# Kernel tuning notes

Measured on AMD Instinct MI355X. Metric: run time of the kernel, lower is better.

## Reference

```python
import jax, jax.numpy as jnp
import numpy as np

DIM = 1024
HEADS = 16
HEAD_DIM = 64
ROT = 32          # rotary_emb_dim = min(max(head_dim//2, 32), head_dim)
BASE = 10000.0
SEQ = 2048
BATCH = 2


def setup_inputs() -> dict:
    key = jax.random.key(0)
    k1, k2, k3, k4 = jax.random.split(key, 4)
    s = 0.02
    return {
        "x": jax.random.normal(k1, (BATCH, SEQ, DIM), dtype=jnp.float32),
        # Linear weights stored as [in, out] (equivalent to torch W^T)
        "w_q": jax.random.normal(k2, (DIM, HEADS * HEAD_DIM), dtype=jnp.float32) * s,
        "w_kv": jax.random.normal(k3, (DIM, 2 * HEADS * HEAD_DIM), dtype=jnp.float32) * s,
        "w_out": jax.random.normal(k4, (HEADS * HEAD_DIM, DIM), dtype=jnp.float32) * s,
    }


def _rotate_half(t):
    # x-transformers style: split last dim in half, (-x2, x1)
    x1, x2 = t[..., : ROT // 2], t[..., ROT // 2 :]
    return jnp.concatenate([-x2, x1], axis=-1)


def _apply_rope(t, cos, sin):
    # rotate only the first ROT dims of head_dim, pass through the rest
    t_rot, t_pass = t[..., :ROT], t[..., ROT:]
    t_rot = t_rot * cos + _rotate_half(t_rot) * sin
    return jnp.concatenate([t_rot, t_pass], axis=-1)


def reference(x, w_q, w_kv, w_out):
    b, n, _ = x.shape
    # QKV projections
    q = (x @ w_q).reshape(b, n, HEADS, HEAD_DIM).transpose(0, 2, 1, 3)  # b h n d
    k, v = jnp.split(x @ w_kv, 2, axis=-1)
    k = k.reshape(b, n, HEADS, HEAD_DIM).transpose(0, 2, 1, 3)
    v = v.reshape(b, n, HEADS, HEAD_DIM).transpose(0, 2, 1, 3)

    # rotary embedding over full kv length (no cache -> k.shape[-2] == n)
    inv_freq = 1.0 / (BASE ** (jnp.arange(0, ROT, 2, dtype=jnp.float32) / ROT))
    freqs = jnp.arange(n, dtype=jnp.float32)[:, None] * inv_freq[None, :]  # [n, ROT/2]
    freqs = jnp.concatenate([freqs, freqs], axis=-1)                        # [n, ROT]
    cos, sin = jnp.cos(freqs), jnp.sin(freqs)
    q = _apply_rope(q, cos, sin)
    k = _apply_rope(k, cos, sin)

    # causal attention
    scale = HEAD_DIM ** -0.5
    scores = jnp.einsum('bhid,bhjd->bhij', q, k) * scale  # [b,h,n,n]
    causal_mask = jnp.tril(jnp.ones((n, n), dtype=bool))
    scores = jnp.where(causal_mask, scores, jnp.finfo(scores.dtype).min)
    attn = jax.nn.softmax(scores, axis=-1)
    out = jnp.einsum('bhij,bhjd->bhid', attn, v)

    out = out.transpose(0, 2, 1, 3).reshape(b, n, HEADS * HEAD_DIM)
    return out @ w_out
```

## Files before the change

### kernel.cpp

```cpp
#include <hip/hip_runtime.h>

typedef unsigned short u16;
typedef unsigned int u32;
typedef __bf16 bf16x8 __attribute__((ext_vector_type(8)));
typedef unsigned short u16x8v __attribute__((ext_vector_type(8)));
typedef unsigned short u16x4v __attribute__((ext_vector_type(4)));
typedef unsigned int u32x4 __attribute__((ext_vector_type(4)));
typedef float f32x4 __attribute__((ext_vector_type(4)));
typedef float f32x16 __attribute__((ext_vector_type(16)));

#define SEQ 2048
#define NH 16
#define HD 64
#define DIMM 1024

__device__ __forceinline__ u16 f2bf(float f) {
  unsigned u = __builtin_bit_cast(unsigned, f);
  u += 0x7fffu + ((u >> 16) & 1u);
  return (u16)(u >> 16);
}
__device__ __forceinline__ float bf2f(u16 b) {
  return __builtin_bit_cast(float, ((unsigned)b) << 16);
}
__device__ __forceinline__ u32 pk2(float a, float b) {
  return (u32)f2bf(a) | ((u32)f2bf(b) << 16);
}

__device__ __forceinline__ void gload16(const u16* g, u16* l) {
  __builtin_amdgcn_global_load_lds(
      (const __attribute__((address_space(1))) unsigned int*)g,
      (__attribute__((address_space(3))) unsigned int*)l, 16, 0, 0);
}

__global__ void conv_x(const float* __restrict__ x, u16* __restrict__ oh) {
  size_t i = (size_t)blockIdx.x * 256 + threadIdx.x;
  f32x4 v = *(const f32x4*)(x + i * 4);
  u16x4v h;
#pragma unroll
  for (int j = 0; j < 4; ++j) h[j] = f2bf(v[j]);
  *(u16x4v*)(oh + i * 4) = h;
}

__global__ void conv_wT(const float* __restrict__ W, u16* __restrict__ Wt,
                        int Kd, int Nd) {
  __shared__ float t[32][33];
  int n0 = blockIdx.x * 32, k0 = blockIdx.y * 32;
  int c = threadIdx.x & 31, r8 = threadIdx.x >> 5;
#pragma unroll
  for (int rr = 0; rr < 32; rr += 8)
    t[r8 + rr][c] = W[(size_t)(k0 + r8 + rr) * Nd + n0 + c];
  __syncthreads();
#pragma unroll
  for (int rr = 0; rr < 32; rr += 8)
    Wt[(size_t)(n0 + r8 + rr) * Kd + k0 + c] = f2bf(t[c][r8 + rr]);
}

__global__ void __launch_bounds__(256, 2)
gemmQKV(const u16* __restrict__ Ah, const u16* __restrict__ Bt,
        u16* __restrict__ Qb, u16* __restrict__ Kb, u16* __restrict__ Vb,
        int M, int N, int K) {
  __shared__ u16 AsH[128][64];
  __shared__ u16 BsH[128][64];
  const int tid = threadIdx.x;
  const int lane = tid & 63, wave = tid >> 6;
  const int wr = wave >> 1, wc = wave & 1;
  const int lr = lane & 15, lg = lane >> 4;
  const int bm = blockIdx.y * 128, bn = blockIdx.x * 128;
  const int lrow = lane >> 3;
  const int lcol8 = (lane & 7) * 8;

  f32x4 acc[4][4];
#pragma unroll
  for (int m = 0; m < 4; ++m)
#pragma unroll
    for (int n = 0; n < 4; ++n) acc[m][n] = (f32x4){0.f, 0.f, 0.f, 0.f};

  for (int k0 = 0; k0 < K; k0 += 64) {
    __syncthreads();
#pragma unroll
    for (int c = 0; c < 4; ++c) {
      int r0 = wave * 32 + c * 8;
      size_t arow = (size_t)(bm + r0 + lrow) * K + k0 + lcol8;
      size_t brow = (size_t)(bn + r0 + lrow) * K + k0 + lcol8;
      gload16(Ah + arow, &AsH[r0][0]);
      gload16(Bt + brow, &BsH[r0][0]);
    }
    __syncthreads();
#pragma unroll
    for (int kk = 0; kk < 2; ++kk) {
      bf16x8 afh[4], bfh[4];
#pragma unroll
      for (int m = 0; m < 4; ++m)
        afh[m] = *(const bf16x8*)&AsH[wr * 64 + m * 16 + lr][kk * 32 + lg * 8];
#pragma unroll
      for (int n = 0; n < 4; ++n)
        bfh[n] = *(const bf16x8*)&BsH[wc * 64 + n * 16 + lr][kk * 32 + lg * 8];
#pragma unroll
      for (int m = 0; m < 4; ++m)
#pragma unroll
        for (int n = 0; n < 4; ++n)
          acc[m][n] = __builtin_amdgcn_mfma_f32_16x16x32_bf16(afh[m], bfh[n],
                                                              acc[m][n], 0, 0, 0);
    }
  }

  const int sel = bn >> 10;
  u16* __restrict__ dst = sel == 0 ? Qb : (sel == 1 ? Kb : Vb);
  if (sel < 2) {
    float inv = __expf(-(float)lr * 0.5756462732485115f);
#pragma unroll
    for (int m = 0; m < 4; ++m) {
#pragma unroll
      for (int r = 0; r < 4; ++r) {
        int row = bm + wr * 64 + m * 16 + 4 * lg + r;
        int s = row & (SEQ - 1);
        float ang = (float)s * inv;
        float sn, cs;
        __sincosf(ang, &sn, &cs);
        float x1 = acc[m][0][r], x2 = acc[m][1][r];
        acc[m][0][r] = x1 * cs - x2 * sn;
        acc[m][1][r] = x2 * cs + x1 * sn;
      }
    }
  }

#pragma unroll
  for (int m = 0; m < 4; ++m) {
#pragma unroll
    for (int n = 0; n < 4; ++n) {
#pragma unroll
      for (int r = 0; r < 4; ++r) {
        int row = bm + wr * 64 + m * 16 + 4 * lg + r;
        int col = bn + wc * 64 + n * 16 + lr;
        int b = row >> 11, s = row & 2047;
        int h = (col >> 6) & 15, d = col & 63;
        dst[(((size_t)(b * NH + h)) * SEQ + s) * HD + d] = f2bf(acc[m][n][r]);
      }
    }
  }
}

__global__ void __launch_bounds__(256, 2)
gemm1(const u16* __restrict__ A, const u16* __restrict__ Bt,
      float* __restrict__ CF, int M, int N, int K) {
  __shared__ u16 As[128][64];
  __shared__ u16 Bs[64][64];
  const int tid = threadIdx.x;
  const int lane = tid & 63, wave = tid >> 6;
  const int wr = wave >> 1, wc = wave & 1;
  const int lr = lane & 15, lg = lane >> 4;
  const int bm = blockIdx.y * 128, bn = blockIdx.x * 64;
  const int lrow = lane >> 3;
  const int lcol8 = (lane & 7) * 8;

  f32x4 acc[4][2];
#pragma unroll
  for (int m = 0; m < 4; ++m)
#pragma unroll
    for (int n = 0; n < 2; ++n) acc[m][n] = (f32x4){0.f, 0.f, 0.f, 0.f};

  for (int k0 = 0; k0 < K; k0 += 64) {
    __syncthreads();
#pragma unroll
    for (int c = 0; c < 4; ++c) {
      int r0 = wave * 32 + c * 8;
      gload16(A + (size_t)(bm + r0 + lrow) * K + k0 + lcol8, &As[r0][0]);
    }
#pragma unroll
    for (int c = 0; c < 2; ++c) {
      int r0 = wave * 16 + c * 8;
      gload16(Bt + (size_t)(bn + r0 + lrow) * K + k0 + lcol8, &Bs[r0][0]);
    }
    __syncthreads();
#pragma unroll
    for (int kk = 0; kk < 2; ++kk) {
      bf16x8 af[4], bfr[2];
#pragma unroll
      for (int m = 0; m < 4; ++m)
        af[m] = *(const bf16x8*)&As[wr * 64 + m * 16 + lr][kk * 32 + lg * 8];
#pragma unroll
      for (int n = 0; n < 2; ++n)
        bfr[n] = *(const bf16x8*)&Bs[wc * 32 + n * 16 + lr][kk * 32 + lg * 8];
#pragma unroll
      for (int m = 0; m < 4; ++m)
#pragma unroll
        for (int n = 0; n < 2; ++n)
          acc[m][n] = __builtin_amdgcn_mfma_f32_16x16x32_bf16(af[m], bfr[n],
                                                              acc[m][n], 0, 0, 0);
    }
  }

#pragma unroll
  for (int m = 0; m < 4; ++m)
#pragma unroll
    for (int n = 0; n < 2; ++n)
#pragma unroll
      for (int r = 0; r < 4; ++r) {
        int row = bm + wr * 64 + m * 16 + 4 * lg + r;
        int col = bn + wc * 32 + n * 16 + lr;
        CF[(size_t)row * N + col] = acc[m][n][r];
      }
}

__global__ void __launch_bounds__(512, 1)
attn_kernel(const u16* __restrict__ Q, const u16* __restrict__ K,
            const u16* __restrict__ V, float* __restrict__ Op0,
            float* __restrict__ Op1, float* __restrict__ ml) {
  __shared__ u16 Ks[2][64][72];
  __shared__ u16 Vt[2][64][72];
  const int tid = threadIdx.x, lane = tid & 63, wave = tid >> 6;
  const int g = wave >> 2, w4 = wave & 3;
  const int hi = lane >> 5, l31 = lane & 31;
  const int tid_g = w4 * 64 + lane;
  const int bx = blockIdx.x, bh = blockIdx.y;
  const size_t kvbase = (size_t)bh * SEQ * HD;
  const int HS = 32 * SEQ;
  const int kr0 = tid_g >> 3, kc0 = (tid_g & 7) * 8;
  const int vr = tid_g & 63;
  const int vc0A = (tid_g >> 6) * 8, vc0B = vc0A + 32;

  u16x8v kreg0, kreg1, vreg0, vreg1;
  float* __restrict__ Opart = g ? Op1 : Op0;

#pragma unroll 1
  for (int phase = 0; phase < 2; ++phase) {
    const int qt = phase ? 15 - bx : bx;
    const int nper = qt + 1;
    const int ktbegin = g * nper;
    const int qrow = qt * 128 + w4 * 32 + l31;

    const u16* qp = Q + kvbase + (size_t)qrow * HD + 8 * hi;
    bf16x8 qf0 = *(const bf16x8*)(qp);
    bf16x8 qf1 = *(const bf16x8*)(qp + 16);
    bf16x8 qf2 = *(const bf16x8*)(qp + 32);
    bf16x8 qf3 = *(const bf16x8*)(qp + 48);

    f32x16 o0 = {0.f}, o1 = {0.f};
    float m = -1e30f, l = 0.f;

    {
      const u16* kp = K + kvbase + (size_t)(ktbegin * 64) * HD;
      const u16* vp = V + kvbase + (size_t)(ktbegin * 64) * HD;
      kreg0 = *(const u16x8v*)(kp + (size_t)kr0 * HD + kc0);
      kreg1 = *(const u16x8v*)(kp + (size_t)(kr0 + 32) * HD + kc0);
      vreg0 = *(const u16x8v*)(vp + (size_t)vr * HD + vc0A);
      vreg1 = *(const u16x8v*)(vp + (size_t)vr * HD + vc0B);
    }

#pragma unroll 1
    for (int i = 0; i < nper; ++i) {
      const int kt = ktbegin + i;
      __syncthreads();
      *(u16x8v*)&Ks[g][kr0][kc0] = kreg0;
      *(u16x8v*)&Ks[g][kr0 + 32][kc0] = kreg1;
#pragma unroll
      for (int j = 0; j < 8; ++j) Vt[g][vc0A + j][vr] = vreg0[j];
#pragma unroll
      for (int j = 0; j < 8; ++j) Vt[g][vc0B + j][vr] = vreg1[j];
      __syncthreads();
      if (i + 1 < nper) {
        const u16* kp = K + kvbase + (size_t)((kt + 1) * 64) * HD;
        const u16* vp = V + kvbase + (size_t)((kt + 1) * 64) * HD;
        kreg0 = *(const u16x8v*)(kp + (size_t)kr0 * HD + kc0);
        kreg1 = *(const u16x8v*)(kp + (size_t)(kr0 + 32) * HD + kc0);
        vreg0 = *(const u16x8v*)(vp + (size_t)vr * HD + vc0A);
        vreg1 = *(const u16x8v*)(vp + (size_t)vr * HD + vc0B);
      }

      f32x16 s0 = {0.f}, s1 = {0.f};
      __builtin_amdgcn_s_setprio(1);
#pragma unroll
      for (int kk = 0; kk < 4; ++kk) {
        bf16x8 qk = kk == 0 ? qf0 : (kk == 1 ? qf1 : (kk == 2 ? qf2 : qf3));
        bf16x8 af0 = *(const bf16x8*)&Ks[g][l31][16 * kk + 8 * hi];
        bf16x8 af1 = *(const bf16x8*)&Ks[g][32 + l31][16 * kk + 8 * hi];
        s0 = __builtin_amdgcn_mfma_f32_32x32x16_bf16(af0, qk, s0, 0, 0, 0);
        s1 = __builtin_amdgcn_mfma_f32_32x32x16_bf16(af1, qk, s1, 0, 0, 0);
      }
      __builtin_amdgcn_s_setprio(0);
      s0 *= 0.125f;
      s1 *= 0.125f;

      if (kt >= 2 * qt) {
#pragma unroll
        for (int r = 0; r < 16; ++r) {
          int rowi = (r & 3) + 8 * (r >> 2) + 4 * hi;
          if (kt * 64 + rowi > qrow) s0[r] = -1e30f;
          if (kt * 64 + 32 + rowi > qrow) s1[r] = -1e30f;
        }
      }

      float mx = s0[0];
#pragma unroll
      for (int r = 1; r < 16; ++r) mx = fmaxf(mx, s0[r]);
#pragma unroll
      for (int r = 0; r < 16; ++r) mx = fmaxf(mx, s1[r]);
      mx = fmaxf(mx, __shfl_xor(mx, 32));

      bool defer = __all(mx - m <= 8.f);
      if (!defer) {
        float mn = fmaxf(m, mx);
        float fac = __expf(m - mn);
        m = mn;
        l *= fac;
        o0 *= fac;
        o1 *= fac;
      }
      float rsum = 0.f;
#pragma unroll
      for (int r = 0; r < 16; ++r) {
        s0[r] = __expf(s0[r] - m);
        rsum += s0[r];
      }
#pragma unroll
      for (int r = 0; r < 16; ++r) {
        s1[r] = __expf(s1[r] - m);
        rsum += s1[r];
      }
      rsum += __shfl_xor(rsum, 32);
      l += rsum;

      u32 P0a[4], P1a[4], P0b[4], P1b[4];
#pragma unroll
      for (int gg = 0; gg < 4; ++gg) {
        P0a[gg] = pk2(s0[4 * gg], s0[4 * gg + 1]);
        P1a[gg] = pk2(s0[4 * gg + 2], s0[4 * gg + 3]);
        P0b[gg] = pk2(s1[4 * gg], s1[4 * gg + 1]);
        P1b[gg] = pk2(s1[4 * gg + 2], s1[4 * gg + 3]);
      }

      __builtin_amdgcn_s_setprio(1);
#pragma unroll
      for (int c = 0; c < 4; ++c) {
        const int gA = 2 * (c & 1);
        u32 p0lo, p0hi, p1lo, p1hi;
        if (c < 2) {
          p0lo = P0a[gA];
          p0hi = P0a[gA + 1];
          p1lo = P1a[gA];
          p1hi = P1a[gA + 1];
        } else {
          p0lo = P0b[gA];
          p0hi = P0b[gA + 1];
          p1lo = P1b[gA];
          p1hi = P1b[gA + 1];
        }
        u32 send0 = hi ? p0lo : p0hi;
        u32 send1 = hi ? p1lo : p1hi;
        u32 recv0 = (u32)__shfl_xor((int)send0, 32);
        u32 recv1 = (u32)__shfl_xor((int)send1, 32);
        u32 own0 = hi ? p0hi : p0lo;
        u32 own1 = hi ? p1hi : p1lo;
        u32x4 bw;
        bw[0] = hi ? recv0 : own0;
        bw[1] = hi ? recv1 : own1;
        bw[2] = hi ? own0 : recv0;
        bw[3] = hi ? own1 : recv1;
        bf16x8 bfrag = __builtin_bit_cast(bf16x8, bw);
        bf16x8 av0 = *(const bf16x8*)&Vt[g][l31][16 * c + 8 * hi];
        bf16x8 av1 = *(const bf16x8*)&Vt[g][32 + l31][16 * c + 8 * hi];
        o0 = __builtin_amdgcn_mfma_f32_32x32x16_bf16(av0, bfrag, o0, 0, 0, 0);
        o1 = __builtin_amdgcn_mfma_f32_32x32x16_bf16(av1, bfrag, o1, 0, 0, 0);
      }
      __builtin_amdgcn_s_setprio(0);
    }

    {
      size_t base = ((size_t)bh * SEQ + qrow) * HD;
#pragma unroll
      for (int gg = 0; gg < 4; ++gg) {
        f32x4 v0 = {o0[4 * gg], o0[4 * gg + 1], o0[4 * gg + 2], o0[4 * gg + 3]};
        f32x4 v1 = {o1[4 * gg], o1[4 * gg + 1], o1[4 * gg + 2], o1[4 * gg + 3]};
        *(f32x4*)(Opart + base + 8 * gg + 4 * hi) = v0;
        *(f32x4*)(Opart + base + 32 + 8 * gg + 4 * hi) = v1;
      }
      if (hi == 0) {
        ml[g * HS + bh * SEQ + qrow] = m;
        ml[2 * HS + g * HS + bh * SEQ + qrow] = l;
      }
    }
    __syncthreads();
  }
}

__global__ void merge_kernel(const float* __restrict__ Op0,
                             const float* __restrict__ Op1,
                             const float* __restrict__ ml,
                             u16* __restrict__ O) {
  int i = blockIdx.x * 256 + threadIdx.x;
  int row = i >> 4;
  int d0 = (i & 15) * 4;
  size_t base = (size_t)row * 64 + d0;
  f32x4 o1 = *(const f32x4*)(Op0 + base);
  f32x4 o2 = *(const f32x4*)(Op1 + base);
  const int HS = 32 * SEQ;
  float m1 = ml[row], m2 = ml[HS + row];
  float l1 = ml[2 * HS + row], l2 = ml[3 * HS + row];
  float M = fmaxf(m1, m2);
  float w1 = __expf(m1 - M), w2 = __expf(m2 - M);
  float inv = 1.0f / (l1 * w1 + l2 * w2);
  int bh = row >> 11, s = row & 2047;
  int b = bh >> 4, h = bh & 15;
  u16x4v rr;
#pragma unroll
  for (int j = 0; j < 4; ++j) rr[j] = f2bf((o1[j] * w1 + o2[j] * w2) * inv);
  *(u16x4v*)(O + ((size_t)(b * SEQ + s)) * DIMM + h * HD + d0) = rr;
}

extern "C" void kernel_launch(void* const* d_in, const int* in_sizes, int n_in,
                              void* d_out, int out_size, void* d_ws, size_t ws_size,
                              hipStream_t stream) {
  const float* x = (const float*)d_in[0];
  const float* wq = (const float*)d_in[1];
  const float* wkv = (const float*)d_in[2];
  const float* wout = (const float*)d_in[3];
  float* out = (float*)d_out;

  u16* ws = (u16*)d_ws;
  const size_t M1 = (size_t)1024 * 1024;
  u16* xh = ws;
  u16* xl = xh + 4 * M1;
  u16* wqTh = xl + 4 * M1;
  u16* wkvTh = wqTh + M1;
  u16* Qb = wkvTh + 2 * M1;
  u16* Kb = Qb + 4 * M1;
  u16* Vb = Kb + 4 * M1;
  float* Op0 = out;
  float* Op1 = (float*)xh;
  float* mlbuf = (float*)wqTh;
  u16* Ob = Qb;
  u16* woutT = Kb;

  conv_x<<<4096, 256, 0, stream>>>(x, xh);
  conv_wT<<<dim3(32, 32), 256, 0, stream>>>(wq, wqTh, 1024, 1024);
  conv_wT<<<dim3(64, 32), 256, 0, stream>>>(wkv, wkvTh, 1024, 2048);

  gemmQKV<<<dim3(24, 32), 256, 0, stream>>>(xh, wqTh, Qb, Kb, Vb,
                                            4096, 3072, 1024);

  attn_kernel<<<dim3(8, 32), 512, 0, stream>>>(Qb, Kb, Vb, Op0, Op1, mlbuf);
  merge_kernel<<<4096, 256, 0, stream>>>(Op0, Op1, mlbuf, Ob);

  conv_wT<<<dim3(32, 32), 256, 0, stream>>>(wout, woutT, 1024, 1024);
  gemm1<<<dim3(16, 32), 256, 0, stream>>>(Ob, woutT, out, 4096, 1024, 1024);
}
```

Measured before the change: 129.7 us.

## Split attention into independent per-half blocks instead of paired-phase 512-thread blocks

The attention kernel used to run 512-thread blocks holding two 4-wave groups, each group covering one half of the KV range, with every block handling two mirrored query tiles in sequence to balance causal work. Now each 256-thread block handles one query tile and one KV half, launched on a 16x2x32 grid with launch bounds allowing 4 blocks per CU. This gives 1024 smaller blocks and lets the hardware scheduler do the balancing and overlap, in place of the manual mirrored-tile pairing. The cost is that the explicit load balancing is dropped, so uneven causal tiles depend on the scheduler, and the tighter launch bound may constrain registers.

```diff
diff --git a/kernel.cpp b/kernel.cpp
--- a/kernel.cpp
+++ b/kernel.cpp
@@ -202,184 +202,176 @@
       }
 }
 
-__global__ void __launch_bounds__(512, 1)
+__global__ void __launch_bounds__(256, 4)
 attn_kernel(const u16* __restrict__ Q, const u16* __restrict__ K,
             const u16* __restrict__ V, float* __restrict__ Op0,
             float* __restrict__ Op1, float* __restrict__ ml) {
-  __shared__ u16 Ks[2][64][72];
-  __shared__ u16 Vt[2][64][72];
+  __shared__ u16 Ks[64][72];
+  __shared__ u16 Vt[64][72];
   const int tid = threadIdx.x, lane = tid & 63, wave = tid >> 6;
-  const int g = wave >> 2, w4 = wave & 3;
   const int hi = lane >> 5, l31 = lane & 31;
-  const int tid_g = w4 * 64 + lane;
-  const int bx = blockIdx.x, bh = blockIdx.y;
+  const int qt = blockIdx.x, g = blockIdx.y, bh = blockIdx.z;
   const size_t kvbase = (size_t)bh * SEQ * HD;
   const int HS = 32 * SEQ;
-  const int kr0 = tid_g >> 3, kc0 = (tid_g & 7) * 8;
-  const int vr = tid_g & 63;
-  const int vc0A = (tid_g >> 6) * 8, vc0B = vc0A + 32;
+  const int kr0 = tid >> 3, kc0 = (tid & 7) * 8;
+  const int vr = tid & 63;
+  const int vc0A = (tid >> 6) * 8, vc0B = vc0A + 32;
+
+  const int nper = qt + 1;
+  const int ktbegin = g * nper;
+  const int qrow = qt * 128 + wave * 32 + l31;
+  float* __restrict__ Opart = g ? Op1 : Op0;
+
+  const u16* qp = Q + kvbase + (size_t)qrow * HD + 8 * hi;
+  bf16x8 qf0 = *(const bf16x8*)(qp);
+  bf16x8 qf1 = *(const bf16x8*)(qp + 16);
+  bf16x8 qf2 = *(const bf16x8*)(qp + 32);
+  bf16x8 qf3 = *(const bf16x8*)(qp + 48);
+
+  f32x16 o0 = {0.f}, o1 = {0.f};
+  float m = -1e30f, l = 0.f;
 
   u16x8v kreg0, kreg1, vreg0, vreg1;
-  float* __restrict__ Opart = g ? Op1 : Op0;
+  {
+    const u16* kp = K + kvbase + (size_t)(ktbegin * 64) * HD;
+    const u16* vp = V + kvbase + (size_t)(ktbegin * 64) * HD;
+    kreg0 = *(const u16x8v*)(kp + (size_t)kr0 * HD + kc0);
+    kreg1 = *(const u16x8v*)(kp + (size_t)(kr0 + 32) * HD + kc0);
+    vreg0 = *(const u16x8v*)(vp + (size_t)vr * HD + vc0A);
+    vreg1 = *(const u16x8v*)(vp + (size_t)vr * HD + vc0B);
+  }
 
 #pragma unroll 1
-  for (int phase = 0; phase < 2; ++phase) {
-    const int qt = phase ? 15 - bx : bx;
-    const int nper = qt + 1;
-    const int ktbegin = g * nper;
-    const int qrow = qt * 128 + w4 * 32 + l31;
-
-    const u16* qp = Q + kvbase + (size_t)qrow * HD + 8 * hi;
-    bf16x8 qf0 = *(const bf16x8*)(qp);
-    bf16x8 qf1 = *(const bf16x8*)(qp + 16);
-    bf16x8 qf2 = *(const bf16x8*)(qp + 32);
-    bf16x8 qf3 = *(const bf16x8*)(qp + 48);
-
-    f32x16 o0 = {0.f}, o1 = {0.f};
-    float m = -1e30f, l = 0.f;
-
-    {
-      const u16* kp = K + kvbase + (size_t)(ktbegin * 64) * HD;
-      const u16* vp = V + kvbase + (size_t)(ktbegin * 64) * HD;
+  for (int i = 0; i < nper; ++i) {
+    const int kt = ktbegin + i;
+    __syncthreads();
+    *(u16x8v*)&Ks[kr0][kc0] = kreg0;
+    *(u16x8v*)&Ks[kr0 + 32][kc0] = kreg1;
+#pragma unroll
+    for (int j = 0; j < 8; ++j) Vt[vc0A + j][vr] = vreg0[j];
+#pragma unroll
+    for (int j = 0; j < 8; ++j) Vt[vc0B + j][vr] = vreg1[j];
+    __syncthreads();
+    if (i + 1 < nper) {
+      const u16* kp = K + kvbase + (size_t)((kt + 1) * 64) * HD;
+      const u16* vp = V + kvbase + (size_t)((kt + 1) * 64) * HD;
       kreg0 = *(const u16x8v*)(kp + (size_t)kr0 * HD + kc0);
       kreg1 = *(const u16x8v*)(kp + (size_t)(kr0 + 32) * HD + kc0);
       vreg0 = *(const u16x8v*)(vp + (size_t)vr * HD + vc0A);
       vreg1 = *(const u16x8v*)(vp + (size_t)vr * HD + vc0B);
     }
 
-#pragma unroll 1
-    for (int i = 0; i < nper; ++i) {
-      const int kt = ktbegin + i;
-      __syncthreads();
-      *(u16x8v*)&Ks[g][kr0][kc0] = kreg0;
-      *(u16x8v*)&Ks[g][kr0 + 32][kc0] = kreg1;
-#pragma unroll
-      for (int j = 0; j < 8; ++j) Vt[g][vc0A + j][vr] = vreg0[j];
-#pragma unroll
-      for (int j = 0; j < 8; ++j) Vt[g][vc0B + j][vr] = vreg1[j];
-      __syncthreads();
-      if (i + 1 < nper) {
-        const u16* kp = K + kvbase + (size_t)((kt + 1) * 64) * HD;
-        const u16* vp = V + kvbase + (size_t)((kt + 1) * 64) * HD;
-        kreg0 = *(const u16x8v*)(kp + (size_t)kr0 * HD + kc0);
-        kreg1 = *(const u16x8v*)(kp + (size_t)(kr0 + 32) * HD + kc0);
-        vreg0 = *(const u16x8v*)(vp + (size_t)vr * HD + vc0A);
-        vreg1 = *(const u16x8v*)(vp + (size_t)vr * HD + vc0B);
+    f32x16 s0 = {0.f}, s1 = {0.f};
+    __builtin_amdgcn_s_setprio(1);
+#pragma unroll
+    for (int kk = 0; kk < 4; ++kk) {
+      bf16x8 qk = kk == 0 ? qf0 : (kk == 1 ? qf1 : (kk == 2 ? qf2 : qf3));
+      bf16x8 af0 = *(const bf16x8*)&Ks[l31][16 * kk + 8 * hi];
+      bf16x8 af1 = *(const bf16x8*)&Ks[32 + l31][16 * kk + 8 * hi];
+      s0 = __builtin_amdgcn_mfma_f32_32x32x16_bf16(af0, qk, s0, 0, 0, 0);
+      s1 = __builtin_amdgcn_mfma_f32_32x32x16_bf16(af1, qk, s1, 0, 0, 0);
+    }
+    __builtin_amdgcn_s_setprio(0);
+    s0 *= 0.125f;
+    s1 *= 0.125f;
+
+    if (kt >= 2 * qt) {
+#pragma unroll
+      for (int r = 0; r < 16; ++r) {
+        int rowi = (r & 3) + 8 * (r >> 2) + 4 * hi;
+        if (kt * 64 + rowi > qrow) s0[r] = -1e30f;
+        if (kt * 64 + 32 + rowi > qrow) s1[r] = -1e30f;
       }
-
-      f32x16 s0 = {0.f}, s1 = {0.f};
-      __builtin_amdgcn_s_setprio(1);
-#pragma unroll
-      for (int kk = 0; kk < 4; ++kk) {
-        bf16x8 qk = kk == 0 ? qf0 : (kk == 1 ? qf1 : (kk == 2 ? qf2 : qf3));
-        bf16x8 af0 = *(const bf16x8*)&Ks[g][l31][16 * kk + 8 * hi];
-        bf16x8 af1 = *(const bf16x8*)&Ks[g][32 + l31][16 * kk + 8 * hi];
-        s0 = __builtin_amdgcn_mfma_f32_32x32x16_bf16(af0, qk, s0, 0, 0, 0);
-        s1 = __builtin_amdgcn_mfma_f32_32x32x16_bf16(af1, qk, s1, 0, 0, 0);
+    }
+
+    float mx = s0[0];
+#pragma unroll
+    for (int r = 1; r < 16; ++r) mx = fmaxf(mx, s0[r]);
+#pragma unroll
+    for (int r = 0; r < 16; ++r) mx = fmaxf(mx, s1[r]);
+    mx = fmaxf(mx, __shfl_xor(mx, 32));
+
+    bool defer = __all(mx - m <= 8.f);
+    if (!defer) {
+      float mn = fmaxf(m, mx);
+      float fac = __expf(m - mn);
+      m = mn;
+      l *= fac;
+      o0 *= fac;
+      o1 *= fac;
+    }
+    float rsum = 0.f;
+#pragma unroll
+    for (int r = 0; r < 16; ++r) {
+      s0[r] = __expf(s0[r] - m);
+      rsum += s0[r];
+    }
+#pragma unroll
+    for (int r = 0; r < 16; ++r) {
+      s1[r] = __expf(s1[r] - m);
+      rsum += s1[r];
+    }
+    rsum += __shfl_xor(rsum, 32);
+    l += rsum;
+
+    u32 P0a[4], P1a[4], P0b[4], P1b[4];
+#pragma unroll
+    for (int gg = 0; gg < 4; ++gg) {
+      P0a[gg] = pk2(s0[4 * gg], s0[4 * gg + 1]);
+      P1a[gg] = pk2(s0[4 * gg + 2], s0[4 * gg + 3]);
+      P0b[gg] = pk2(s1[4 * gg], s1[4 * gg + 1]);
+      P1b[gg] = pk2(s1[4 * gg + 2], s1[4 * gg + 3]);
+    }
+
+    __builtin_amdgcn_s_setprio(1);
+#pragma unroll
+    for (int c = 0; c < 4; ++c) {
+      const int gA = 2 * (c & 1);
+      u32 p0lo, p0hi, p1lo, p1hi;
+      if (c < 2) {
+        p0lo = P0a[gA];
+        p0hi = P0a[gA + 1];
+        p1lo = P1a[gA];
+        p1hi = P1a[gA + 1];
+      } else {
+        p0lo = P0b[gA];
+        p0hi = P0b[gA + 1];
+        p1lo = P1b[gA];
+        p1hi = P1b[gA + 1];
       }
-      __builtin_amdgcn_s_setprio(0);
-      s0 *= 0.125f;
-      s1 *= 0.125f;
-
-      if (kt >= 2 * qt) {
-#pragma unroll
-        for (int r = 0; r < 16; ++r) {
-          int rowi = (r & 3) + 8 * (r >> 2) + 4 * hi;
-          if (kt * 64 + rowi > qrow) s0[r] = -1e30f;
-          if (kt * 64 + 32 + rowi > qrow) s1[r] = -1e30f;
-        }
-      }
-
-      float mx = s0[0];
-#pragma unroll
-      for (int r = 1; r < 16; ++r) mx = fmaxf(mx, s0[r]);
-#pragma unroll
-      for (int r = 0; r < 16; ++r) mx = fmaxf(mx, s1[r]);
-      mx = fmaxf(mx, __shfl_xor(mx, 32));
-
-      bool defer = __all(mx - m <= 8.f);
-      if (!defer) {
-        float mn = fmaxf(m, mx);
-        float fac = __expf(m - mn);
-        m = mn;
-        l *= fac;
-        o0 *= fac;
-        o1 *= fac;
-      }
-      float rsum = 0.f;
-#pragma unroll
-      for (int r = 0; r < 16; ++r) {
-        s0[r] = __expf(s0[r] - m);
-        rsum += s0[r];
-      }
-#pragma unroll
-      for (int r = 0; r < 16; ++r) {
-        s1[r] = __expf(s1[r] - m);
-        rsum += s1[r];
-      }
-      rsum += __shfl_xor(rsum, 32);
-      l += rsum;
-
-      u32 P0a[4], P1a[4], P0b[4], P1b[4];
-#pragma unroll
-      for (int gg = 0; gg < 4; ++gg) {
-        P0a[gg] = pk2(s0[4 * gg], s0[4 * gg + 1]);
-        P1a[gg] = pk2(s0[4 * gg + 2], s0[4 * gg + 3]);
-        P0b[gg] = pk2(s1[4 * gg], s1[4 * gg + 1]);
-        P1b[gg] = pk2(s1[4 * gg + 2], s1[4 * gg + 3]);
-      }
-
-      __builtin_amdgcn_s_setprio(1);
-#pragma unroll
-      for (int c = 0; c < 4; ++c) {
-        const int gA = 2 * (c & 1);
-        u32 p0lo, p0hi, p1lo, p1hi;
-        if (c < 2) {
-          p0lo = P0a[gA];
-          p0hi = P0a[gA + 1];
-          p1lo = P1a[gA];
-          p1hi = P1a[gA + 1];
-        } else {
-          p0lo = P0b[gA];
-          p0hi = P0b[gA + 1];
-          p1lo = P1b[gA];
-          p1hi = P1b[gA + 1];
-        }
-        u32 send0 = hi ? p0lo : p0hi;
-        u32 send1 = hi ? p1lo : p1hi;
-        u32 recv0 = (u32)__shfl_xor((int)send0, 32);
-        u32 recv1 = (u32)__shfl_xor((int)send1, 32);
-        u32 own0 = hi ? p0hi : p0lo;
-        u32 own1 = hi ? p1hi : p1lo;
-        u32x4 bw;
-        bw[0] = hi ? recv0 : own0;
-        bw[1] = hi ? recv1 : own1;
-        bw[2] = hi ? own0 : recv0;
-        bw[3] = hi ? own1 : recv1;
-        bf16x8 bfrag = __builtin_bit_cast(bf16x8, bw);
-        bf16x8 av0 = *(const bf16x8*)&Vt[g][l31][16 * c + 8 * hi];
-        bf16x8 av1 = *(const bf16x8*)&Vt[g][32 + l31][16 * c + 8 * hi];
-        o0 = __builtin_amdgcn_mfma_f32_32x32x16_bf16(av0, bfrag, o0, 0, 0, 0);
-        o1 = __builtin_amdgcn_mfma_f32_32x32x16_bf16(av1, bfrag, o1, 0, 0, 0);
-      }
-      __builtin_amdgcn_s_setprio(0);
-    }
-
-    {
-      size_t base = ((size_t)bh * SEQ + qrow) * HD;
-#pragma unroll
-      for (int gg = 0; gg < 4; ++gg) {
-        f32x4 v0 = {o0[4 * gg], o0[4 * gg + 1], o0[4 * gg + 2], o0[4 * gg + 3]};
-        f32x4 v1 = {o1[4 * gg], o1[4 * gg + 1], o1[4 * gg + 2], o1[4 * gg + 3]};
-        *(f32x4*)(Opart + base + 8 * gg + 4 * hi) = v0;
-        *(f32x4*)(Opart + base + 32 + 8 * gg + 4 * hi) = v1;
-      }
-      if (hi == 0) {
-        ml[g * HS + bh * SEQ + qrow] = m;
-        ml[2 * HS + g * HS + bh * SEQ + qrow] = l;
-      }
-    }
-    __syncthreads();
+      u32 send0 = hi ? p0lo : p0hi;
+      u32 send1 = hi ? p1lo : p1hi;
+      u32 recv0 = (u32)__shfl_xor((int)send0, 32);
+      u32 recv1 = (u32)__shfl_xor((int)send1, 32);
+      u32 own0 = hi ? p0hi : p0lo;
+      u32 own1 = hi ? p1hi : p1lo;
+      u32x4 bw;
+      bw[0] = hi ? recv0 : own0;
+      bw[1] = hi ? recv1 : own1;
+      bw[2] = hi ? own0 : recv0;
+      bw[3] = hi ? own1 : recv1;
+      bf16x8 bfrag = __builtin_bit_cast(bf16x8, bw);
+      bf16x8 av0 = *(const bf16x8*)&Vt[l31][16 * c + 8 * hi];
+      bf16x8 av1 = *(const bf16x8*)&Vt[32 + l31][16 * c + 8 * hi];
+      o0 = __builtin_amdgcn_mfma_f32_32x32x16_bf16(av0, bfrag, o0, 0, 0, 0);
+      o1 = __builtin_amdgcn_mfma_f32_32x32x16_bf16(av1, bfrag, o1, 0, 0, 0);
+    }
+    __builtin_amdgcn_s_setprio(0);
+  }
+
+  {
+    size_t base = ((size_t)bh * SEQ + qrow) * HD;
+#pragma unroll
+    for (int gg = 0; gg < 4; ++gg) {
+      f32x4 v0 = {o0[4 * gg], o0[4 * gg + 1], o0[4 * gg + 2], o0[4 * gg + 3]};
+      f32x4 v1 = {o1[4 * gg], o1[4 * gg + 1], o1[4 * gg + 2], o1[4 * gg + 3]};
+      *(f32x4*)(Opart + base + 8 * gg + 4 * hi) = v0;
+      *(f32x4*)(Opart + base + 32 + 8 * gg + 4 * hi) = v1;
+    }
+    if (hi == 0) {
+      ml[g * HS + bh * SEQ + qrow] = m;
+      ml[2 * HS + g * HS + bh * SEQ + qrow] = l;
+    }
   }
 }
 
@@ -438,7 +430,7 @@
   gemmQKV<<<dim3(24, 32), 256, 0, stream>>>(xh, wqTh, Qb, Kb, Vb,
                                             4096, 3072, 1024);
 
-  attn_kernel<<<dim3(8, 32), 512, 0, stream>>>(Qb, Kb, Vb, Op0, Op1, mlbuf);
+  attn_kernel<<<dim3(16, 2, 32), 256, 0, stream>>>(Qb, Kb, Vb, Op0, Op1, mlbuf);
   merge_kernel<<<4096, 256, 0, stream>>>(Op0, Op1, mlbuf, Ob);
 
   conv_wT<<<dim3(32, 32), 256, 0, stream>>>(wout, woutT, 1024, 1024);
```

New measurement: 150.4 us. 1.16x slower.
